# Performance work log

Hardware: AMD Instinct MI355X
Metric: run time of the kernel (lower is better)

The kernel has to match this reference:

```python
import jax, jax.numpy as jnp
import numpy as np

NV, NA, T, FD, C, E = 192, 64, 128, 1024, 128, 262144
SPK = 3
N = (NV + NA) * T  # 32768 total graph nodes
NEG = -1e30


def _seg_max(msg, dst, mask):
    # masked scatter-max; PyG fills segments with no messages with 0
    m = jnp.where(mask[:, None], msg, NEG)
    out = jax.ops.segment_max(m, dst, num_segments=N)
    return jnp.where(out > NEG * 0.5, out, 0.0)


def _edge_conv(x, src, dst, mask, W1, b1, W2, b2):
    # EdgeConv: max_j MLP(cat[x_i, x_j - x_i])
    xi = x[dst]
    h = jnp.concatenate([xi, x[src] - xi], axis=-1)  # [E, 2C]
    h = jax.nn.relu(h @ W1 + b1) @ W2 + b2
    return _seg_max(h, dst, mask)


def _sage_conv(x, src, dst, mask, Wl, bl, Wr):
    # SAGEConv: lin_l(mean_j x_j) + lin_r(x_i), lin_r has no bias
    mf = mask.astype(x.dtype)
    s = jax.ops.segment_sum(x[src] * mf[:, None], dst, num_segments=N)
    cnt = jax.ops.segment_sum(mf, dst, num_segments=N)
    mean = s / jnp.maximum(cnt, 1.0)[:, None]
    return mean @ Wl + bl + x @ Wr


def setup_inputs():
    ks = jax.random.split(jax.random.key(0), 24)
    s = 0.05
    vals = jnp.array([-3, -2, -1, 0, 1, 3], jnp.int32)
    return {
        "x_visual": jax.random.normal(ks[0], (NV, T, FD), jnp.float32),
        "x_audio": jax.random.normal(ks[1], (NA, T, FD), jnp.float32),
        "W011": jax.random.normal(ks[2], (FD, C)) * s, "b011": jnp.zeros((C,)),
        "W012": jax.random.normal(ks[3], (FD, C)) * s, "b012": jnp.zeros((C,)),
        "ecA_W1": jax.random.normal(ks[4], (2 * C, C)) * s, "ecA_b1": jnp.zeros((C,)),
        "ecA_W2": jax.random.normal(ks[5], (C, C)) * s, "ecA_b2": jnp.zeros((C,)),
        "ec1_W1": jax.random.normal(ks[6], (2 * C, C)) * s, "ec1_b1": jnp.zeros((C,)),
        "ec1_W2": jax.random.normal(ks[7], (C, C)) * s, "ec1_b2": jnp.zeros((C,)),
        "ec2_W1": jax.random.normal(ks[8], (2 * C, C)) * s, "ec2_b1": jnp.zeros((C,)),
        "ec2_W2": jax.random.normal(ks[9], (C, C)) * s, "ec2_b2": jnp.zeros((C,)),
        "ec3_W1": jax.random.normal(ks[10], (2 * C, C)) * s, "ec3_b1": jnp.zeros((C,)),
        "ec3_W2": jax.random.normal(ks[11], (C, C)) * s, "ec3_b2": jnp.zeros((C,)),
        "sage_Wl": jax.random.normal(ks[12], (C, C)) * s, "sage_bl": jnp.zeros((C,)),
        "sage_Wr": jax.random.normal(ks[13], (C, C)) * s,
        "fc_W": jax.random.normal(ks[14], (C, 1)) * s, "fc_b": jnp.zeros((1,)),
        "edge_index": jax.random.randint(ks[15], (2, E), 0, N, dtype=jnp.int32),
        "edge_attr": vals[jax.random.randint(ks[16], (E,), 0, 6)],
        "speakers": SPK,
    }


def reference(x_visual, x_audio, W011, b011, W012, b012,
              ecA_W1, ecA_b1, ecA_W2, ecA_b2,
              ec1_W1, ec1_b1, ec1_W2, ec1_b2,
              ec2_W1, ec2_b1, ec2_W2, ec2_b2,
              ec3_W1, ec3_b1, ec3_W2, ec3_b2,
              sage_Wl, sage_bl, sage_Wr, fc_W, fc_b,
              edge_index, edge_attr, speakers):
    xv = x_visual @ W011 + b011          # [NV, T, C]
    xa = x_audio @ W012 + b012           # [NA, T, C]
    x = jnp.concatenate([xv, xa], axis=0).reshape(-1, C)  # [N, C]
    src, dst = edge_index[0], edge_index[1]
    m_audio = edge_attr == -2
    m_vpa = edge_attr == -3
    m_acv = edge_attr == 3
    m1 = (edge_attr >= 0) & (edge_attr <= 1)
    m2 = (edge_attr <= 0) & (edge_attr >= -1)
    m3 = jnp.abs(edge_attr) <= 1
    # Visual_Add_Audio_GNN: max-aggregate (x_i + x_j)
    xa_g = jax.nn.relu(_seg_max(x[dst] + x[src], dst, m_vpa))
    a = jax.nn.relu(_edge_conv(xa_g, src, dst, m_audio, ecA_W1, ecA_b1, ecA_W2, ecA_b2))
    a_res = a @ fc_W + fc_b              # [N, 1] per-node audio scores
    # Audio_Weight_Add_Visual_GNN: sum-aggregate (w_j * x_j + x_i)
    wmsg = jnp.where(m_acv[:, None], a_res[src] * x[src] + x[dst], 0.0)
    xv2 = jax.nn.relu(jax.ops.segment_sum(wmsg, dst, num_segments=N))

    def branch(mask, W1, b1, W2, b2):
        h = jax.nn.relu(_edge_conv(xv2, src, dst, mask, W1, b1, W2, b2))
        return jax.nn.relu(_sage_conv(h, src, dst, mask, sage_Wl, sage_bl, sage_Wr))

    xo = (branch(m1, ec1_W1, ec1_b1, ec1_W2, ec1_b2)
          + branch(m2, ec2_W1, ec2_b1, ec2_W2, ec2_b2)
          + branch(m3, ec3_W1, ec3_b1, ec3_W2, ec3_b2))
    # gather main-speaker visual nodes
    idx = (jnp.arange(0, NV * T, speakers * T)[:, None] + jnp.arange(T)).reshape(-1)
    return xo[idx]
```

## Files before the change

### kernel.cpp

```cpp
#include <hip/hip_runtime.h>
#include <cstdint>
#include <cstddef>

#define NVv 192
#define NAa 64
#define TT 128
#define FDd 1024
#define CCc 128
#define EEe 262144
#define NNn 32768

typedef _Float16 f16x8 __attribute__((ext_vector_type(8)));
typedef float f32x4 __attribute__((ext_vector_type(4)));

#define CAP0 65536
#define CAP1 65536
#define CAP2 65536
#define CAP3 98304
#define CAP4 98304
#define CAP5 147456
#define ARENA_TOTAL (CAP0+CAP1+CAP2+CAP3+CAP4+CAP5)
#define OFF0 0
#define OFF1 CAP0
#define OFF2 (CAP0+CAP1)
#define OFF3 (CAP0+CAP1+CAP2)
#define OFF4 (CAP0+CAP1+CAP2+CAP3)
#define OFF5 (CAP0+CAP1+CAP2+CAP3+CAP4)

#define MPAD 136

__device__ __forceinline__ void eval_masks(int a, bool m[6]) {
    m[0] = (a == -3); m[1] = (a == -2); m[2] = (a == 3);
    m[3] = (a >= 0) & (a <= 1);
    m[4] = (a >= -1) & (a <= 0);
    m[5] = (a >= -1) & (a <= 1);
}

struct WSmall { const float* p[14]; };
struct PV3  { const _Float16* Wd[3]; const _Float16* Wv[3]; const float* b1[3];
              _Float16* P[3]; _Float16* V[3]; };
struct MLP3 { const _Float16* W2[3]; const float* b2[3];
              const _Float16* P[3]; const _Float16* V[3]; float* AH[3]; };

__global__ __launch_bounds__(256) void k_setup(
    const float* __restrict__ W011, const float* __restrict__ W012,
    WSmall wsm, _Float16* __restrict__ WT, _Float16* __restrict__ WTs,
    float* __restrict__ hf)
{
    int blk = blockIdx.x, tid = threadIdx.x;
    if (blk < 1024) {
        int idx = blk * 256 + tid;
        int which = idx >> 17;
        int r = idx & 131071;
        int n = r >> 10, k = r & 1023;
        const float* src = which ? W012 : W011;
        WT[idx] = (_Float16)src[k * 128 + n];
    } else if (blk < 1920) {
        int idx = (blk - 1024) * 256 + tid;
        int seg = idx >> 14;
        int r = idx & 16383;
        int n = r >> 7, k = r & 127;
        const float* src = wsm.p[seg];
        float v = src[k * 128 + n];
        if (seg < 12 && (seg % 3) == 0) v -= src[16384 + k * 128 + n];
        WTs[idx] = (_Float16)v;
    } else {
        size_t i = (size_t)(blk - 1920) * 1024 + (size_t)tid * 4;
        *(float4*)(hf + i) = make_float4(0.f, 0.f, 0.f, 0.f);
    }
}

__global__ __launch_bounds__(256) void k_hist(
    const int* __restrict__ attr, const int* __restrict__ edst,
    int* __restrict__ hist)
{
    int e = blockIdx.x * 256 + threadIdx.x;
    int a = attr[e], d = edst[e];
    bool m[6]; eval_masks(a, m);
#pragma unroll
    for (int j = 0; j < 6; ++j)
        if (m[j]) atomicAdd(&hist[j * NNn + d], 1);
}

__global__ __launch_bounds__(256) void k_scan_a(
    const int* __restrict__ hist, int* __restrict__ base, int* __restrict__ bsum)
{
    __shared__ int wsum[4];
    int idx = blockIdx.x * 256 + threadIdx.x;
    int tid = threadIdx.x, lane = tid & 63, wv = tid >> 6;
    int v = hist[idx];
    int x = v;
#pragma unroll
    for (int off = 1; off < 64; off <<= 1) {
        int y = __shfl_up(x, off, 64);
        if (lane >= off) x += y;
    }
    if (lane == 63) wsum[wv] = x;
    __syncthreads();
    int add = 0;
    for (int w = 0; w < wv; ++w) add += wsum[w];
    base[idx] = add + x - v;
    if (tid == 255) bsum[blockIdx.x] = add + x;
}

__global__ __launch_bounds__(384) void k_scan_b(int* __restrict__ bsum, int* __restrict__ cnts)
{
    int wv = threadIdx.x >> 6;
    int lane = threadIdx.x & 63;
    int run = 0;
#pragma unroll
    for (int c0 = 0; c0 < 128; c0 += 64) {
        int v = bsum[wv * 128 + c0 + lane];
        int x = v;
#pragma unroll
        for (int off = 1; off < 64; off <<= 1) {
            int y = __shfl_up(x, off, 64);
            if (lane >= off) x += y;
        }
        bsum[wv * 128 + c0 + lane] = run + (x - v);
        run += __shfl(x, 63, 64);
    }
    if (lane == 0) cnts[wv] = run;
}

__global__ __launch_bounds__(256) void k_scan_c(int* __restrict__ base, const int* __restrict__ bsum)
{
    base[blockIdx.x * 256 + threadIdx.x] += bsum[blockIdx.x];
}

__global__ __launch_bounds__(256) void k_fill_zero(
    const int* __restrict__ esrc, const int* __restrict__ edst,
    const int* __restrict__ attr, const int* __restrict__ base,
    int* __restrict__ fill, int2* __restrict__ arena, const int* __restrict__ hist,
    float* __restrict__ AH0, float* __restrict__ AH1,
    float* __restrict__ AH2, float* __restrict__ AH3)
{
    int blk = blockIdx.x, tid = threadIdx.x;
    if (blk < 1024) {
        int e = blk * 256 + tid;
        int a = attr[e];
        int s = esrc[e], d = edst[e];
        bool m[6]; eval_masks(a, m);
        const int caps[6] = {CAP0, CAP1, CAP2, CAP3, CAP4, CAP5};
        const int offs[6] = {OFF0, OFF1, OFF2, OFF3, OFF4, OFF5};
#pragma unroll
        for (int j = 0; j < 6; ++j) {
            if (m[j]) {
                int pos = base[j * NNn + d] + atomicAdd(&fill[j * NNn + d], 1);
                if (pos < caps[j]) arena[offs[j] + pos] = make_int2(s, d);
            }
        }
    } else {
        int zb = blk - 1024;
        int col = tid & 127, sub = tid >> 7;
        const int js[4] = {1, 3, 4, 5};
        float* AHs[4] = {AH0, AH1, AH2, AH3};
        for (int d = zb * 2 + sub; d < NNn; d += 2048 * 2) {
#pragma unroll
            for (int jj = 0; jj < 4; ++jj) {
                int j = js[jj];
                int c = hist[j * NNn + d];
                bool need;
                if (c == 0) need = true;
                else {
                    int b = base[j * NNn + d], e = b + c;
                    need = ((b & 63) == 0) || ((e & 63) == 0) || ((b >> 6) != ((e - 1) >> 6));
                }
                if (need) AHs[jj][(size_t)d * 128 + col] = 0.f;
            }
        }
    }
}

__global__ __launch_bounds__(512) void k_proj(
    const float* __restrict__ xv, const float* __restrict__ xa,
    const _Float16* __restrict__ BTv, const _Float16* __restrict__ BTa,
    float* __restrict__ Pp0, float* __restrict__ Pp1)
{
    __shared__ _Float16 Bl[2][128][136];
    const int tid = threadIdx.x, wave = tid >> 6, lane = tid & 63;
    const int tile = blockIdx.x >> 1, kh = blockIdx.x & 1;
    const float* A; const _Float16* BT; int mbase, obase;
    if (tile < 192) { A = xv; BT = BTv; mbase = tile * 128; obase = mbase; }
    else { A = xa; BT = BTa; mbase = (tile - 192) * 128; obase = 24576 + mbase; }
    float* Pout = kh ? Pp1 : Pp0;
    const int kbase = kh * 512;

    const int mrow = mbase + wave * 16 + (lane & 15);
    const int fk   = (lane >> 4) * 8;
    f32x4 acc[8];
#pragma unroll
    for (int i = 0; i < 8; ++i) acc[i] = (f32x4){0,0,0,0};

#pragma unroll
    for (int it = 0; it < 4; ++it) {
        int c = it * 512 + tid;
        int n = c >> 4, koff = (c & 15) * 8;
        *(f16x8*)&Bl[0][n][koff] = *(const f16x8*)(BT + (size_t)n * 1024 + kbase + koff);
    }
    f16x8 af[4];
#pragma unroll
    for (int t4 = 0; t4 < 4; ++t4) {
        const float* asrc = A + (size_t)mrow * 1024 + kbase + t4 * 32 + fk;
        float4 a0 = *(const float4*)asrc;
        float4 a1 = *(const float4*)(asrc + 4);
        af[t4] = (f16x8){ (_Float16)a0.x, (_Float16)a0.y, (_Float16)a0.z, (_Float16)a0.w,
                          (_Float16)a1.x, (_Float16)a1.y, (_Float16)a1.z, (_Float16)a1.w };
    }
    __syncthreads();

    for (int kc = 0; kc < 4; ++kc) {
        const int cur = kc & 1;
        f16x8 nf[4];
        if (kc < 3) {
            const int nxt = cur ^ 1;
#pragma unroll
            for (int it = 0; it < 4; ++it) {
                int c = it * 512 + tid;
                int n = c >> 4, koff = (c & 15) * 8;
                *(f16x8*)&Bl[nxt][n][koff] =
                    *(const f16x8*)(BT + (size_t)n * 1024 + kbase + (kc + 1) * 128 + koff);
            }
#pragma unroll
            for (int t4 = 0; t4 < 4; ++t4) {
                const float* asrc = A + (size_t)mrow * 1024 + kbase + (kc + 1) * 128 + t4 * 32 + fk;
                float4 a0 = *(const float4*)asrc;
                float4 a1 = *(const float4*)(asrc + 4);
                nf[t4] = (f16x8){ (_Float16)a0.x, (_Float16)a0.y, (_Float16)a0.z, (_Float16)a0.w,
                                  (_Float16)a1.x, (_Float16)a1.y, (_Float16)a1.z, (_Float16)a1.w };
            }
        }
#pragma unroll
        for (int t4 = 0; t4 < 4; ++t4)
#pragma unroll
            for (int nt = 0; nt < 8; ++nt) {
                f16x8 bf = *(const f16x8*)&Bl[cur][nt * 16 + (lane & 15)][t4 * 32 + fk];
                acc[nt] = __builtin_amdgcn_mfma_f32_16x16x32_f16(af[t4], bf, acc[nt], 0, 0, 0);
            }
        if (kc < 3) {
#pragma unroll
            for (int t4 = 0; t4 < 4; ++t4) af[t4] = nf[t4];
        }
        __syncthreads();
    }
    const int cbase = lane & 15, rloc = (lane >> 4) * 4;
    const int wgrp = wave & 3;
    float* Hsf = (float*)&Bl[0][0][0] + (size_t)wgrp * 16 * 132;
#pragma unroll
    for (int grp = 0; grp < 2; ++grp) {
        if ((wave >> 2) == grp) {
#pragma unroll
            for (int nt = 0; nt < 8; ++nt) {
                int c2 = nt * 16 + cbase;
#pragma unroll
                for (int rr = 0; rr < 4; ++rr)
                    Hsf[(rloc + rr) * 132 + c2] = acc[nt][rr];
            }
#pragma unroll
            for (int it = 0; it < 8; ++it) {
                int id = it * 64 + lane;
                int row = id >> 5, off = (id & 31) * 4;
                float4 v = *(float4*)&Hsf[row * 132 + off];
                *(float4*)&Pout[(size_t)(obase + wave * 16 + row) * 128 + off] = v;
            }
        }
        __syncthreads();
    }
}

__global__ __launch_bounds__(256) void k_reduce(
    const float* __restrict__ Pp0, const float* __restrict__ Pp1,
    const float* __restrict__ b011, const float* __restrict__ b012,
    float* __restrict__ X)
{
    size_t f = (size_t)blockIdx.x * 256 + threadIdx.x;
    size_t i = f * 4;
    int col = (int)(i & 127);
    int row = (int)(i >> 7);
    const float* bias = (row < 24576) ? b011 : b012;
    float4 a = *(const float4*)(Pp0 + i);
    float4 b = *(const float4*)(Pp1 + i);
    float4 bb = *(const float4*)(bias + col);
    *(float4*)(X + i) = make_float4(a.x + b.x + bb.x, a.y + b.y + bb.y,
                                    a.z + b.z + bb.z, a.w + b.w + bb.w);
}

__device__ __forceinline__ void pv_body(
    const float* __restrict__ A, const _Float16* __restrict__ BT1,
    const float* __restrict__ b1, const _Float16* __restrict__ BT2,
    _Float16* __restrict__ P, _Float16* __restrict__ V, int tileblk,
    _Float16 (*Bl1)[136], _Float16 (*Bl2)[136], float* bb)
{
    const int tid = threadIdx.x, wave = tid >> 6, lane = tid & 63;
    const int r0 = tileblk * 64 + wave * 16;
    const int fk = (lane >> 4) * 8;
    const int mrow = r0 + (lane & 15);
    float4 a0[4], a1[4];
#pragma unroll
    for (int t4 = 0; t4 < 4; ++t4) {
        const float* asrc = A + (size_t)mrow * 128 + t4 * 32 + fk;
        a0[t4] = *(const float4*)asrc;
        a1[t4] = *(const float4*)(asrc + 4);
    }
#pragma unroll
    for (int it = 0; it < 8; ++it) {
        int c = it * 256 + tid;
        int n = c >> 4, koff = (c & 15) * 8;
        *(f16x8*)&Bl1[n][koff] = *(const f16x8*)(BT1 + (size_t)n * 128 + koff);
        *(f16x8*)&Bl2[n][koff] = *(const f16x8*)(BT2 + (size_t)n * 128 + koff);
    }
    if (tid < 128) bb[tid] = b1[tid];
    __syncthreads();

    f16x8 af[4];
#pragma unroll
    for (int t4 = 0; t4 < 4; ++t4)
        af[t4] = (f16x8){ (_Float16)a0[t4].x, (_Float16)a0[t4].y, (_Float16)a0[t4].z, (_Float16)a0[t4].w,
                          (_Float16)a1[t4].x, (_Float16)a1[t4].y, (_Float16)a1[t4].z, (_Float16)a1[t4].w };
    f32x4 acc1[8], acc2[8];
#pragma unroll
    for (int i = 0; i < 8; ++i) { acc1[i] = (f32x4){0,0,0,0}; acc2[i] = (f32x4){0,0,0,0}; }
#pragma unroll
    for (int t4 = 0; t4 < 4; ++t4)
#pragma unroll
        for (int nt = 0; nt < 8; ++nt) {
            f16x8 bf1 = *(const f16x8*)&Bl1[nt * 16 + (lane & 15)][t4 * 32 + fk];
            f16x8 bf2 = *(const f16x8*)&Bl2[nt * 16 + (lane & 15)][t4 * 32 + fk];
            acc1[nt] = __builtin_amdgcn_mfma_f32_16x16x32_f16(af[t4], bf1, acc1[nt], 0, 0, 0);
            acc2[nt] = __builtin_amdgcn_mfma_f32_16x16x32_f16(af[t4], bf2, acc2[nt], 0, 0, 0);
        }
    __syncthreads();
    _Float16* Hs = &Bl1[0][0] + (size_t)wave * 16 * 136;
    const int cbase = lane & 15, rloc = (lane >> 4) * 4;
#pragma unroll
    for (int nt = 0; nt < 8; ++nt) {
        int c2 = nt * 16 + cbase;
        float bvv = bb[c2];
#pragma unroll
        for (int rr = 0; rr < 4; ++rr)
            Hs[(rloc + rr) * 136 + c2] = (_Float16)(acc1[nt][rr] + bvv);
    }
#pragma unroll
    for (int it = 0; it < 4; ++it) {
        int id = it * 64 + lane;
        int row = id >> 4, koff = (id & 15) * 8;
        *(f16x8*)&P[(size_t)(r0 + row) * 128 + koff] = *(f16x8*)&Hs[row * 136 + koff];
    }
#pragma unroll
    for (int nt = 0; nt < 8; ++nt) {
        int c2 = nt * 16 + cbase;
#pragma unroll
        for (int rr = 0; rr < 4; ++rr)
            Hs[(rloc + rr) * 136 + c2] = (_Float16)acc2[nt][rr];
    }
#pragma unroll
    for (int it = 0; it < 4; ++it) {
        int id = it * 64 + lane;
        int row = id >> 4, koff = (id & 15) * 8;
        *(f16x8*)&V[(size_t)(r0 + row) * 128 + koff] = *(f16x8*)&Hs[row * 136 + koff];
    }
}

__global__ __launch_bounds__(256) void k_pv(
    const float* __restrict__ A, const _Float16* __restrict__ BT1,
    const float* __restrict__ b1, const _Float16* __restrict__ BT2,
    _Float16* __restrict__ P, _Float16* __restrict__ V)
{
    __shared__ _Float16 Bl1[128][136];
    __shared__ _Float16 Bl2[128][136];
    __shared__ float bb[128];
    pv_body(A, BT1, b1, BT2, P, V, blockIdx.x, Bl1, Bl2, bb);
}

__global__ __launch_bounds__(256) void k_pv3(const float* __restrict__ A, PV3 p)
{
    __shared__ _Float16 Bl1[128][136];
    __shared__ _Float16 Bl2[128][136];
    __shared__ float bb[128];
    int b = blockIdx.x >> 9, t = blockIdx.x & 511;
    pv_body(A, p.Wd[b], p.b1[b], p.Wv[b], p.P[b], p.V[b], t, Bl1, Bl2, bb);
}

__device__ __forceinline__ void mlp_loadW(
    const _Float16* __restrict__ W2T, const float* __restrict__ b2,
    _Float16 (*W2l)[MPAD], float* __restrict__ b2l)
{
    int tid = threadIdx.x;
#pragma unroll
    for (int i = 0; i < 4; ++i) {
        int c = tid + i * 512;
        int n = c >> 4, koff = (c & 15) * 8;
        *(f16x8*)&W2l[n][koff] = *(const f16x8*)(W2T + n * 128 + koff);
    }
    if (tid < 128) b2l[tid] = b2[tid];
}

__device__ __forceinline__ void mlp_tile2(
    const _Float16* __restrict__ P, const _Float16* __restrict__ V,
    const int2* __restrict__ list, int cnt, int t, float* __restrict__ agg,
    _Float16 (*Rl)[MPAD], const _Float16 (*W2l)[MPAD], const float* __restrict__ b2l,
    int2* __restrict__ eSD, unsigned char* __restrict__ gstart,
    int* __restrict__ gdst, int* __restrict__ ngrS)
{
    const int tid  = threadIdx.x & 255;
    const int wave = tid >> 6;
    const int lane = threadIdx.x & 63;
    if (tid < 64) {
        int e = t * 64 + tid;
        eSD[tid] = (e < cnt) ? list[e] : make_int2(0, -1);
    }
    __syncthreads();
    if (tid < 64) {
        int d = eSD[tid].y;
        bool flag = (tid == 0) || (d != eSD[tid - 1].y);
        unsigned long long bm = __ballot(flag);
        int rank = (int)__popcll(bm & ((1ull << tid) - 1ull));
        if (flag) { gstart[rank] = (unsigned char)tid; gdst[rank] = d; }
        if (tid == 0) {
            int ng = (int)__popcll(bm);
            *ngrS = ng;
            gstart[ng] = 64;
        }
    }
    const int rrow = tid >> 4;
    const int rch  = (tid & 15) * 8;
#pragma unroll
    for (int p = 0; p < 4; ++p) {
        int i = p * 16 + rrow;
        int2 sd = eSD[i];
        f16x8 rv = {0, 0, 0, 0, 0, 0, 0, 0};
        if (sd.y >= 0) {
            f16x8 pv = *(const f16x8*)(P + (size_t)sd.y * 128 + rch);
            f16x8 vv = *(const f16x8*)(V + (size_t)sd.x * 128 + rch);
            rv = pv + vv;
#pragma unroll
            for (int q = 0; q < 8; ++q)
                rv[q] = (rv[q] > (_Float16)0.f) ? rv[q] : (_Float16)0.f;
        }
        *(f16x8*)&Rl[i][rch] = rv;
    }
    __syncthreads();

    const int frow  = wave * 16 + (lane & 15);
    const int fq    = (lane >> 4) * 8;
    f32x4 acc[8];
#pragma unroll
    for (int i = 0; i < 8; ++i) acc[i] = (f32x4){0,0,0,0};
#pragma unroll
    for (int t4 = 0; t4 < 4; ++t4) {
        f16x8 af = *(const f16x8*)&Rl[frow][t4 * 32 + fq];
#pragma unroll
        for (int nt = 0; nt < 8; ++nt) {
            f16x8 bf = *(const f16x8*)&W2l[nt * 16 + (lane & 15)][t4 * 32 + fq];
            acc[nt] = __builtin_amdgcn_mfma_f32_16x16x32_f16(af, bf, acc[nt], 0, 0, 0);
        }
    }
    __syncthreads();
    const int rbase = wave * 16 + (lane >> 4) * 4;
    const int cbase = lane & 15;
#pragma unroll
    for (int nt = 0; nt < 8; ++nt) {
        int c2 = nt * 16 + cbase;
        float bv = b2l[c2];
#pragma unroll
        for (int rr = 0; rr < 4; ++rr) {
            int row = rbase + rr;
            Rl[row][c2 ^ (((row >> 3) & 1) << 4)] = (_Float16)fmaxf(acc[nt][rr] + bv, 0.f);
        }
    }
    __syncthreads();
    const int col  = tid & 127;
    const int half = tid >> 7;
    int ng = *ngrS;
    for (int g = half; g < ng; g += 2) {
        int s = gstart[g], e = gstart[g + 1];
        int d = gdst[g];
        if (d < 0) continue;
        float m = 0.f;
        for (int i = s; i < e; ++i)
            m = fmaxf(m, (float)Rl[i][col ^ (((i >> 3) & 1) << 4)]);
        size_t o = (size_t)d * 128 + col;
        if (s == 0 || e == 64)
            atomicMax((unsigned int*)&agg[o], __float_as_uint(m));
        else
            agg[o] = m;
    }
}

__global__ __launch_bounds__(512, 2) void k_edge_mlp(
    const _Float16* __restrict__ P, const _Float16* __restrict__ V,
    const _Float16* __restrict__ W2T, const float* __restrict__ b2,
    const int2* __restrict__ list, const int* __restrict__ cntp, int cap,
    float* __restrict__ agg)
{
    __shared__ _Float16 W2l[128][MPAD];
    __shared__ float b2l[128];
    __shared__ _Float16 Rl[2][64][MPAD];
    __shared__ int2 eSD[2][64];
    __shared__ unsigned char gstart[2][68];
    __shared__ int gdst[2][64];
    __shared__ int ngrS[2];
    int cnt = min(*cntp, cap);
    int ntiles = (cnt + 63) >> 6;
    if ((int)blockIdx.x * 2 >= ntiles) return;
    mlp_loadW(W2T, b2, W2l, b2l);
    const int team = threadIdx.x >> 8;
    for (int base = blockIdx.x * 2; base < ntiles; base += gridDim.x * 2) {
        mlp_tile2(P, V, list, cnt, base + team, agg,
                  Rl[team], W2l, b2l, eSD[team], gstart[team], gdst[team], &ngrS[team]);
    }
}

#define MLP3_G0 146
#define MLP3_G1 146
#define MLP3_G2 220
#define MLP3_GRID (MLP3_G0 + MLP3_G1 + MLP3_G2)

__global__ __launch_bounds__(512, 2) void k_edge_mlp3(
    MLP3 p, const int2* __restrict__ arena, const int* __restrict__ cnts)
{
    __shared__ _Float16 W2l[128][MPAD];
    __shared__ float b2l[128];
    __shared__ _Float16 Rl[2][64][MPAD];
    __shared__ int2 eSD[2][64];
    __shared__ unsigned char gstart[2][68];
    __shared__ int gdst[2][64];
    __shared__ int ngrS[2];
    const int caps[3] = {CAP3, CAP4, CAP5};
    const int offs[3] = {OFF3, OFF4, OFF5};
    int blk = blockIdx.x;
    int b, i, G;
    if (blk < MLP3_G0)                 { b = 0; i = blk;                       G = MLP3_G0; }
    else if (blk < MLP3_G0 + MLP3_G1)  { b = 1; i = blk - MLP3_G0;             G = MLP3_G1; }
    else                               { b = 2; i = blk - (MLP3_G0 + MLP3_G1); G = MLP3_G2; }
    int cnt = min(cnts[3 + b], caps[b]);
    int ntiles = (cnt + 63) >> 6;
    if (i * 2 >= ntiles) return;
    mlp_loadW(p.W2[b], p.b2[b], W2l, b2l);
    const int team = threadIdx.x >> 8;
    const int2* list = arena + offs[b];
    for (int base = i * 2; base < ntiles; base += G * 2) {
        mlp_tile2(p.P[b], p.V[b], list, cnt, base + team, p.AH[b],
                  Rl[team], W2l, b2l, eSD[team], gstart[team], gdst[team], &ngrS[team]);
    }
}

__global__ __launch_bounds__(256) void k_csr_vpa(
    const float* __restrict__ X, const int2* __restrict__ list,
    const int* __restrict__ base, const int* __restrict__ cntarr, int cap,
    float* __restrict__ S)
{
    int col = threadIdx.x & 127;
    int sub = threadIdx.x >> 7;
    for (int d = blockIdx.x * 2 + sub; d < NNn; d += gridDim.x * 2) {
        int c = cntarr[d];
        float v = 0.f;
        if (c > 0) {
            int b = base[d];
            int end = min(b + c, cap);
            float mx = -3.0e38f;
            for (int i = b; i < end; ++i)
                mx = fmaxf(mx, X[(size_t)list[i].x * 128 + col]);
            v = fmaxf(X[(size_t)d * 128 + col] + mx, 0.f);
        }
        S[(size_t)d * 128 + col] = v;
    }
}

__global__ __launch_bounds__(256) void k_csr_acv(
    const float* __restrict__ X, const float* __restrict__ ares,
    const int2* __restrict__ list,
    const int* __restrict__ base, const int* __restrict__ cntarr, int cap,
    float* __restrict__ S)
{
    int col = threadIdx.x & 127;
    int sub = threadIdx.x >> 7;
    for (int d = blockIdx.x * 2 + sub; d < NNn; d += gridDim.x * 2) {
        int c = cntarr[d];
        float v = 0.f;
        if (c > 0) {
            int b = base[d];
            int end = min(b + c, cap);
            float s = 0.f;
            for (int i = b; i < end; ++i) {
                int sr = list[i].x;
                s += ares[sr] * X[(size_t)sr * 128 + col];
            }
            v = fmaxf(s + (float)c * X[(size_t)d * 128 + col], 0.f);
        }
        S[(size_t)d * 128 + col] = v;
    }
}

__global__ __launch_bounds__(256) void k_meanc3(
    float* const AH1, float* const AH2, float* const AH3,
    const int2* __restrict__ arena,
    const int* __restrict__ base, const int* __restrict__ hist,
    const int* __restrict__ spk, int ntarg,
    float* __restrict__ S1c, float* __restrict__ AHc)
{
    int col = threadIdx.x & 127;
    int sub = threadIdx.x >> 7;
    int step = spk[0] * TT;
    const int caps[3] = {CAP3, CAP4, CAP5};
    const int offs[3] = {OFF3, OFF4, OFF5};
    const float* AHs[3] = {AH1, AH2, AH3};
    int total = 3 * ntarg;
    for (int ci2 = blockIdx.x * 2 + sub; ci2 < total; ci2 += gridDim.x * 2) {
        int b = ci2 / ntarg;
        int ci = ci2 - b * ntarg;
        int j = 3 + b;
        const float* AH = AHs[b];
        const int2* list = arena + offs[b];
        int d = (ci >> 7) * step + (ci & 127);
        int c = hist[j * NNn + d];
        float v = 0.f;
        if (c > 0) {
            int bs = base[j * NNn + d];
            int end = min(bs + c, caps[b]);
            float s = 0.f;
            for (int i = bs; i < end; ++i)
                s += AH[(size_t)list[i].x * 128 + col];
            v = s / (float)c;
        }
        S1c[(size_t)ci2 * 128 + col] = v;
        AHc[(size_t)ci2 * 128 + col] = AH[(size_t)d * 128 + col];
    }
}

__global__ __launch_bounds__(256) void k_fc(
    const float* __restrict__ A, const float* __restrict__ W,
    const float* __restrict__ b, float* __restrict__ ares)
{
    int node = blockIdx.x * 4 + (threadIdx.x >> 6);
    int lane = threadIdx.x & 63;
    const float* row = A + (size_t)node * 128;
    float v = row[lane] * W[lane] + row[lane + 64] * W[lane + 64];
#pragma unroll
    for (int off = 32; off > 0; off >>= 1) v += __shfl_down(v, off, 64);
    if (lane == 0) ares[node] = v + b[0];
}

__global__ __launch_bounds__(256) void k_sage_out(
    const float* __restrict__ S1c, const float* __restrict__ AHc,
    const _Float16* __restrict__ WlT, const _Float16* __restrict__ WrT,
    const float* __restrict__ bl, float* __restrict__ out, int ntarg)
{
    __shared__ _Float16 Al[64][40];
    __shared__ _Float16 Bl[128][40];
    const int tid  = threadIdx.x;
    const int wave = tid >> 6;
    const int lane = tid & 63;
    const int m0   = blockIdx.x * 64;

    f32x4 accB[8], accO[8];
#pragma unroll
    for (int i = 0; i < 8; ++i) { accB[i] = (f32x4){0,0,0,0}; accO[i] = (f32x4){0,0,0,0}; }

    const int ar = tid >> 2;
    const int ak = (tid & 3) * 8;
    const int fr = wave * 16 + (lane & 15);
    const int fk = (lane >> 4) * 8;
    const int rbase = wave * 16 + (lane >> 4) * 4;
    const int cbase = lane & 15;

    for (int seg = 0; seg < 6; ++seg) {
        int b = seg >> 1, which = seg & 1;
        const float* A = (which ? AHc : S1c) + (size_t)b * ntarg * 128;
        const _Float16* BT = which ? WrT : WlT;
        for (int k0 = 0; k0 < 128; k0 += 32) {
            __syncthreads();
            const float* asrc = A + (size_t)(m0 + ar) * 128 + (k0 + ak);
            float4 a0 = *(const float4*)asrc;
            float4 a1 = *(const float4*)(asrc + 4);
            f16x8 av = { (_Float16)a0.x, (_Float16)a0.y, (_Float16)a0.z, (_Float16)a0.w,
                         (_Float16)a1.x, (_Float16)a1.y, (_Float16)a1.z, (_Float16)a1.w };
            *(f16x8*)&Al[ar][ak] = av;
#pragma unroll
            for (int i = 0; i < 2; ++i) {
                int c = tid + i * 256;
                int n = c >> 2, koff = (c & 3) * 8;
                *(f16x8*)&Bl[n][koff] = *(const f16x8*)(BT + (size_t)n * 128 + k0 + koff);
            }
            __syncthreads();
            f16x8 af = *(const f16x8*)&Al[fr][fk];
#pragma unroll
            for (int nt = 0; nt < 8; ++nt) {
                f16x8 bf = *(const f16x8*)&Bl[nt * 16 + (lane & 15)][fk];
                accB[nt] = __builtin_amdgcn_mfma_f32_16x16x32_f16(af, bf, accB[nt], 0, 0, 0);
            }
        }
        if (which) {
#pragma unroll
            for (int nt = 0; nt < 8; ++nt) {
                int col = nt * 16 + cbase;
                float bv = bl[col];
#pragma unroll
                for (int rr = 0; rr < 4; ++rr) {
                    accO[nt][rr] += fmaxf(accB[nt][rr] + bv, 0.f);
                    accB[nt][rr] = 0.f;
                }
            }
        }
    }
#pragma unroll
    for (int nt = 0; nt < 8; ++nt) {
        int col = nt * 16 + cbase;
#pragma unroll
        for (int rr = 0; rr < 4; ++rr)
            out[(size_t)(m0 + rbase + rr) * 128 + col] = accO[nt][rr];
    }
}

extern "C" void kernel_launch(void* const* d_in, const int* in_sizes, int n_in,
                              void* d_out, int out_size, void* d_ws, size_t ws_size,
                              hipStream_t stream)
{
    (void)in_sizes; (void)n_in; (void)ws_size;
    const float* xv   = (const float*)d_in[0];
    const float* xa   = (const float*)d_in[1];
    const float* W011 = (const float*)d_in[2];
    const float* b011 = (const float*)d_in[3];
    const float* W012 = (const float*)d_in[4];
    const float* b012 = (const float*)d_in[5];
    const float* ecW1[4] = {(const float*)d_in[6],  (const float*)d_in[10],
                            (const float*)d_in[14], (const float*)d_in[18]};
    const float* ecb1[4] = {(const float*)d_in[7],  (const float*)d_in[11],
                            (const float*)d_in[15], (const float*)d_in[19]};
    const float* ecW2[4] = {(const float*)d_in[8],  (const float*)d_in[12],
                            (const float*)d_in[16], (const float*)d_in[20]};
    const float* ecb2[4] = {(const float*)d_in[9],  (const float*)d_in[13],
                            (const float*)d_in[17], (const float*)d_in[21]};
    const float* sageWl = (const float*)d_in[22];
    const float* sagebl = (const float*)d_in[23];
    const float* sageWr = (const float*)d_in[24];
    const float* fcW    = (const float*)d_in[25];
    const float* fcb    = (const float*)d_in[26];
    const int*   esrc   = (const int*)d_in[27];
    const int*   edst   = esrc + EEe;
    const int*   attr   = (const int*)d_in[28];
    const int*   spk    = (const int*)d_in[29];
    float* out = (float*)d_out;
    const int ntarg = out_size >> 7;

    const size_t NC = (size_t)NNn * CCc;
    float* ws   = (float*)d_ws;
    float* X    = ws;
    float* S1   = ws + 1 * NC;
    float* XV2  = ws + 2 * NC;
    float* AHc  = ws + 3 * NC;
    float* AH0  = ws + 4 * NC;
    float* AH1  = ws + 5 * NC;
    float* AH2  = ws + 6 * NC;
    float* AH3  = ws + 7 * NC;
    _Float16* P0 = (_Float16*)(ws + 8 * NC);
    _Float16* V0 = P0 + NC;
    _Float16* P1 = (_Float16*)X;
    _Float16* V1 = P1 + NC;
    _Float16* P2 = (_Float16*)AHc;
    _Float16* V2 = P2 + NC;
    float* ARES = ws + 9 * NC;
    int*   cnts = (int*)(ARES + NNn);
    int*   bsum = cnts + 16;
    int*   hist = bsum + 1024;
    int*   fill = hist + 6 * NNn;
    int*   base = fill + 6 * NNn;
    int2*  arena = (int2*)(base + 6 * NNn);
    _Float16* WT = (_Float16*)(arena + ARENA_TOTAL);

    const _Float16* W011T = WT;
    const _Float16* W012T = WT + 131072;
    _Float16* WTs = WT + 262144;
    const _Float16* WlT   = WTs + 12 * 16384;
    const _Float16* WrT   = WTs + 13 * 16384;

    WSmall wsm;
    for (int i = 0; i < 4; ++i) {
        wsm.p[3*i + 0] = ecW1[i];
        wsm.p[3*i + 1] = ecW1[i] + 16384;
        wsm.p[3*i + 2] = ecW2[i];
    }
    wsm.p[12] = sageWl; wsm.p[13] = sageWr;
    k_setup<<<2304, 256, 0, stream>>>(W011, W012, wsm, WT, WTs, (float*)hist);
    k_hist<<<EEe / 256, 256, 0, stream>>>(attr, edst, hist);
    k_scan_a<<<768, 256, 0, stream>>>(hist, base, bsum);
    k_scan_b<<<1, 384, 0, stream>>>(bsum, cnts);
    k_scan_c<<<768, 256, 0, stream>>>(base, bsum);
    k_fill_zero<<<3072, 256, 0, stream>>>(esrc, edst, attr, base, fill, arena, hist,
                                          AH0, AH1, AH2, AH3);

    k_proj<<<512, 512, 0, stream>>>(xv, xa, W011T, W012T, S1, XV2);
    k_reduce<<<(int)(NC / 1024), 256, 0, stream>>>(S1, XV2, b011, b012, X);
    k_csr_vpa<<<2048, 256, 0, stream>>>(X, arena + OFF0, base + 0 * NNn,
                                        hist + 0 * NNn, CAP0, S1);
    k_pv<<<512, 256, 0, stream>>>(S1, WTs, ecb1[0], WTs + 16384, P0, V0);
    k_edge_mlp<<<512, 512, 0, stream>>>(P0, V0, WTs + 2 * 16384, ecb2[0],
                                        arena + OFF1, cnts + 1, CAP1, AH0);
    k_fc<<<NNn / 4, 256, 0, stream>>>(AH0, fcW, fcb, ARES);
    k_csr_acv<<<2048, 256, 0, stream>>>(X, ARES, arena + OFF2, base + 2 * NNn,
                                        hist + 2 * NNn, CAP2, XV2);
    PV3 pv3;
    MLP3 m3;
    _Float16* Pb[3] = {P0, P1, P2};
    _Float16* Vb[3] = {V0, V1, V2};
    float* AHb[3] = {AH1, AH2, AH3};
    for (int b = 0; b < 3; ++b) {
        _Float16* Wd = WTs + (3 * (b + 1)) * 16384;
        pv3.Wd[b] = Wd; pv3.Wv[b] = Wd + 16384; pv3.b1[b] = ecb1[b + 1];
        pv3.P[b] = Pb[b]; pv3.V[b] = Vb[b];
        m3.W2[b] = Wd + 2 * 16384; m3.b2[b] = ecb2[b + 1];
        m3.P[b] = Pb[b]; m3.V[b] = Vb[b]; m3.AH[b] = AHb[b];
    }
    k_pv3<<<1536, 256, 0, stream>>>(XV2, pv3);
    k_edge_mlp3<<<MLP3_GRID, 512, 0, stream>>>(m3, arena, cnts);
    k_meanc3<<<2048, 256, 0, stream>>>(AH1, AH2, AH3, arena, base, hist,
                                       spk, ntarg, S1, AHc);
    k_sage_out<<<ntarg / 64, 256, 0, stream>>>(S1, AHc, WlT, WrT, sagebl, out, ntarg);
}
```

Measured before the change: 515.7 us.

## Drop split-K in input projection and fuse bias epilogue into GEMM

The projection GEMM no longer splits K into two halves that write partial sums to scratch buffers for a separate reduce kernel. Each block now covers 64 rows over the full K=1024, adds the bias in the epilogue and writes X directly, so the k_reduce launch and the round trip through two 16 MB partial buffers go away. It also shrinks blocks to 256 threads with a single-buffered B tile to allow more blocks per CU. The cost is a longer serial K loop per block with two barriers per step and no double-buffering of B, and each B tile is now loaded by twice as many blocks.

Measured after the change: 532.4 us. 3.2% more time.

```diff
diff --git a/kernel.cpp b/kernel.cpp
--- a/kernel.cpp
+++ b/kernel.cpp
@@ -172,19 +172,19 @@
     }
 }
 
-__global__ __launch_bounds__(512) void k_proj(
+__global__ __launch_bounds__(256, 4) void k_proj(
     const float* __restrict__ xv, const float* __restrict__ xa,
     const _Float16* __restrict__ BTv, const _Float16* __restrict__ BTa,
-    float* __restrict__ Pp0, float* __restrict__ Pp1)
-{
-    __shared__ _Float16 Bl[2][128][136];
+    const float* __restrict__ b011, const float* __restrict__ b012,
+    float* __restrict__ X)
+{
+    __shared__ _Float16 Bl[128][136];
     const int tid = threadIdx.x, wave = tid >> 6, lane = tid & 63;
-    const int tile = blockIdx.x >> 1, kh = blockIdx.x & 1;
-    const float* A; const _Float16* BT; int mbase, obase;
-    if (tile < 192) { A = xv; BT = BTv; mbase = tile * 128; obase = mbase; }
-    else { A = xa; BT = BTa; mbase = (tile - 192) * 128; obase = 24576 + mbase; }
-    float* Pout = kh ? Pp1 : Pp0;
-    const int kbase = kh * 512;
+    const int tile = blockIdx.x;
+    const float* A; const _Float16* BT; const float* bias; int mbase, obase;
+    if (tile < 384) { A = xv; BT = BTv; bias = b011; mbase = tile * 64; obase = mbase; }
+    else { A = xa; BT = BTa; bias = b012; mbase = (tile - 384) * 64;
+           obase = 24576 + (tile - 384) * 64; }
 
     const int mrow = mbase + wave * 16 + (lane & 15);
     const int fk   = (lane >> 4) * 8;
@@ -192,97 +192,66 @@
 #pragma unroll
     for (int i = 0; i < 8; ++i) acc[i] = (f32x4){0,0,0,0};
 
-#pragma unroll
-    for (int it = 0; it < 4; ++it) {
-        int c = it * 512 + tid;
-        int n = c >> 4, koff = (c & 15) * 8;
-        *(f16x8*)&Bl[0][n][koff] = *(const f16x8*)(BT + (size_t)n * 1024 + kbase + koff);
-    }
-    f16x8 af[4];
-#pragma unroll
-    for (int t4 = 0; t4 < 4; ++t4) {
-        const float* asrc = A + (size_t)mrow * 1024 + kbase + t4 * 32 + fk;
-        float4 a0 = *(const float4*)asrc;
-        float4 a1 = *(const float4*)(asrc + 4);
-        af[t4] = (f16x8){ (_Float16)a0.x, (_Float16)a0.y, (_Float16)a0.z, (_Float16)a0.w,
-                          (_Float16)a1.x, (_Float16)a1.y, (_Float16)a1.z, (_Float16)a1.w };
-    }
+#define STAGE_B(kc_) {                                                          \
+    _Pragma("unroll")                                                           \
+    for (int it = 0; it < 8; ++it) {                                            \
+        int c = it * 256 + tid;                                                 \
+        int n = c >> 4, koff = (c & 15) * 8;                                    \
+        *(f16x8*)&Bl[n][koff] = *(const f16x8*)(BT + (size_t)n * 1024 + (kc_) * 128 + koff); \
+    } }
+
+#define LOAD_A(kc_, dst_) {                                                     \
+    _Pragma("unroll")                                                           \
+    for (int t4 = 0; t4 < 4; ++t4) {                                            \
+        const float* asrc = A + (size_t)mrow * 1024 + (kc_) * 128 + t4 * 32 + fk; \
+        float4 a0 = *(const float4*)asrc;                                       \
+        float4 a1 = *(const float4*)(asrc + 4);                                 \
+        dst_[t4] = (f16x8){ (_Float16)a0.x, (_Float16)a0.y, (_Float16)a0.z, (_Float16)a0.w, \
+                            (_Float16)a1.x, (_Float16)a1.y, (_Float16)a1.z, (_Float16)a1.w }; \
+    } }
+
+    f16x8 af[4], nf[4];
+    STAGE_B(0);
+    LOAD_A(0, af);
     __syncthreads();
 
-    for (int kc = 0; kc < 4; ++kc) {
-        const int cur = kc & 1;
-        f16x8 nf[4];
-        if (kc < 3) {
-            const int nxt = cur ^ 1;
-#pragma unroll
-            for (int it = 0; it < 4; ++it) {
-                int c = it * 512 + tid;
-                int n = c >> 4, koff = (c & 15) * 8;
-                *(f16x8*)&Bl[nxt][n][koff] =
-                    *(const f16x8*)(BT + (size_t)n * 1024 + kbase + (kc + 1) * 128 + koff);
-            }
-#pragma unroll
-            for (int t4 = 0; t4 < 4; ++t4) {
-                const float* asrc = A + (size_t)mrow * 1024 + kbase + (kc + 1) * 128 + t4 * 32 + fk;
-                float4 a0 = *(const float4*)asrc;
-                float4 a1 = *(const float4*)(asrc + 4);
-                nf[t4] = (f16x8){ (_Float16)a0.x, (_Float16)a0.y, (_Float16)a0.z, (_Float16)a0.w,
-                                  (_Float16)a1.x, (_Float16)a1.y, (_Float16)a1.z, (_Float16)a1.w };
-            }
-        }
+    for (int kc = 0; kc < 8; ++kc) {
+        if (kc < 7) LOAD_A(kc + 1, nf);
 #pragma unroll
         for (int t4 = 0; t4 < 4; ++t4)
 #pragma unroll
             for (int nt = 0; nt < 8; ++nt) {
-                f16x8 bf = *(const f16x8*)&Bl[cur][nt * 16 + (lane & 15)][t4 * 32 + fk];
+                f16x8 bf = *(const f16x8*)&Bl[nt * 16 + (lane & 15)][t4 * 32 + fk];
                 acc[nt] = __builtin_amdgcn_mfma_f32_16x16x32_f16(af[t4], bf, acc[nt], 0, 0, 0);
             }
-        if (kc < 3) {
+        __syncthreads();
+        if (kc < 7) {
+            STAGE_B(kc + 1);
 #pragma unroll
             for (int t4 = 0; t4 < 4; ++t4) af[t4] = nf[t4];
-        }
-        __syncthreads();
-    }
+            __syncthreads();
+        }
+    }
+#undef STAGE_B
+#undef LOAD_A
+
+    float* Hsf = (float*)&Bl[0][0] + (size_t)wave * 16 * 132;
     const int cbase = lane & 15, rloc = (lane >> 4) * 4;
-    const int wgrp = wave & 3;
-    float* Hsf = (float*)&Bl[0][0][0] + (size_t)wgrp * 16 * 132;
-#pragma unroll
-    for (int grp = 0; grp < 2; ++grp) {
-        if ((wave >> 2) == grp) {
-#pragma unroll
-            for (int nt = 0; nt < 8; ++nt) {
-                int c2 = nt * 16 + cbase;
-#pragma unroll
-                for (int rr = 0; rr < 4; ++rr)
-                    Hsf[(rloc + rr) * 132 + c2] = acc[nt][rr];
-            }
-#pragma unroll
-            for (int it = 0; it < 8; ++it) {
-                int id = it * 64 + lane;
-                int row = id >> 5, off = (id & 31) * 4;
-                float4 v = *(float4*)&Hsf[row * 132 + off];
-                *(float4*)&Pout[(size_t)(obase + wave * 16 + row) * 128 + off] = v;
-            }
-        }
-        __syncthreads();
-    }
-}
-
-__global__ __launch_bounds__(256) void k_reduce(
-    const float* __restrict__ Pp0, const float* __restrict__ Pp1,
-    const float* __restrict__ b011, const float* __restrict__ b012,
-    float* __restrict__ X)
-{
-    size_t f = (size_t)blockIdx.x * 256 + threadIdx.x;
-    size_t i = f * 4;
-    int col = (int)(i & 127);
-    int row = (int)(i >> 7);
-    const float* bias = (row < 24576) ? b011 : b012;
-    float4 a = *(const float4*)(Pp0 + i);
-    float4 b = *(const float4*)(Pp1 + i);
-    float4 bb = *(const float4*)(bias + col);
-    *(float4*)(X + i) = make_float4(a.x + b.x + bb.x, a.y + b.y + bb.y,
-                                    a.z + b.z + bb.z, a.w + b.w + bb.w);
+#pragma unroll
+    for (int nt = 0; nt < 8; ++nt) {
+        int c2 = nt * 16 + cbase;
+        float bv = bias[c2];
+#pragma unroll
+        for (int rr = 0; rr < 4; ++rr)
+            Hsf[(rloc + rr) * 132 + c2] = acc[nt][rr] + bv;
+    }
+#pragma unroll
+    for (int it = 0; it < 8; ++it) {
+        int id = it * 64 + lane;
+        int row = id >> 5, off = (id & 31) * 4;
+        float4 v = *(float4*)&Hsf[row * 132 + off];
+        *(float4*)&X[(size_t)(obase + wave * 16 + row) * 128 + off] = v;
+    }
 }
 
 __device__ __forceinline__ void pv_body(
@@ -789,8 +758,7 @@
     k_fill_zero<<<3072, 256, 0, stream>>>(esrc, edst, attr, base, fill, arena, hist,
                                           AH0, AH1, AH2, AH3);
 
-    k_proj<<<512, 512, 0, stream>>>(xv, xa, W011T, W012T, S1, XV2);
-    k_reduce<<<(int)(NC / 1024), 256, 0, stream>>>(S1, XV2, b011, b012, X);
+    k_proj<<<512, 256, 0, stream>>>(xv, xa, W011T, W012T, b011, b012, X);
     k_csr_vpa<<<2048, 256, 0, stream>>>(X, arena + OFF0, base + 0 * NNn,
                                         hist + 0 * NNn, CAP0, S1);
     k_pv<<<512, 256, 0, stream>>>(S1, WTs, ecb1[0], WTs + 16384, P0, V0);
```
